# Kernel optimization log

Hardware: AMD Instinct MI355X
Metric: run time of the kernel (lower is better)

## Reference

```python
import jax, jax.numpy as jnp
import numpy as np

EPS = 1e-5

def _bn(x, g, b):
    # training-mode BatchNorm1d over the batch axis (axis 0), biased variance
    m = jnp.mean(x, axis=0)
    v = jnp.var(x, axis=0)
    return g * (x - m) / jnp.sqrt(v + EPS) + b

def _mlp(x, w1, b1, g1, be1, w2, b2, g2, be2, w3, b3):
    # Linear -> BN -> ReLU -> Linear -> BN -> ReLU -> Linear
    x = jax.nn.relu(_bn(x @ w1.T + b1, g1, be1))
    x = jax.nn.relu(_bn(x @ w2.T + b2, g2, be2))
    return x @ w3.T + b3

def setup_inputs() -> dict:
    key = jax.random.key(0)
    ks = jax.random.split(key, 10)
    B, S, D = 256, 512, 128
    w = lambda k: jax.random.normal(k, (D, D), jnp.float32) * 0.05
    return {
        "s": jax.random.normal(ks[0], (B, S, D), jnp.float32),
        "c": jax.random.normal(ks[1], (B, D), jnp.float32),
        "s_w1": w(ks[2]), "s_b1": jnp.zeros((D,), jnp.float32),
        "s_g1": jnp.ones((D,), jnp.float32), "s_be1": jnp.zeros((D,), jnp.float32),
        "s_w2": w(ks[3]), "s_b2": jnp.zeros((D,), jnp.float32),
        "s_g2": jnp.ones((D,), jnp.float32), "s_be2": jnp.zeros((D,), jnp.float32),
        "s_w3": w(ks[4]), "s_b3": jnp.zeros((D,), jnp.float32),
        "c_w1": w(ks[5]), "c_b1": jnp.zeros((D,), jnp.float32),
        "c_g1": jnp.ones((D,), jnp.float32), "c_be1": jnp.zeros((D,), jnp.float32),
        "c_w2": w(ks[6]), "c_b2": jnp.zeros((D,), jnp.float32),
        "c_g2": jnp.ones((D,), jnp.float32), "c_be2": jnp.zeros((D,), jnp.float32),
        "c_w3": w(ks[7]), "c_b3": jnp.zeros((D,), jnp.float32),
    }

def reference(s, c,
              s_w1, s_b1, s_g1, s_be1, s_w2, s_b2, s_g2, s_be2, s_w3, s_b3,
              c_w1, c_b1, c_g1, c_be1, c_w2, c_b2, c_g2, c_be2, c_w3, c_b3):
    # c_mlp: [B, D] -> [B, D] (BN over batch)
    c_out = _mlp(c, c_w1, c_b1, c_g1, c_be1, c_w2, c_b2, c_g2, c_be2, c_w3, c_b3)
    # s_mlp applied per sequence slice; BN stats over batch axis 0 only
    # (matches the torch loop where each s[:, i, :] gets its own BN stats).
    # s: [B, S, D]; _bn with axis=0 gives per-(slice, feature) stats.
    s_h = _mlp(s, s_w1, s_b1, s_g1, s_be1, s_w2, s_b2, s_g2, s_be2, s_w3, s_b3)
    s_out = s_h * c_out[:, None, :]          # context gate, [B, S, D]
    aggregated_c = jnp.max(s_out, axis=1)    # pooling == 'max', [B, D]
    return (s_out, aggregated_c)
```

## Files before the change

### kernel.cpp

```cpp
#include <hip/hip_runtime.h>
#include <hip/hip_bf16.h>
#include <math.h>

#define BATCH 256
#define SEQ   512
#define DIM   128
#define LDSK  136
#define LDSF  132

typedef __attribute__((ext_vector_type(8))) __bf16  bf16x8;
typedef __attribute__((ext_vector_type(4))) __bf16  bf16x4;
typedef __attribute__((ext_vector_type(4))) float   f32x4;

template<int RT>
__device__ __forceinline__ void matmul_layer(
    const __bf16* __restrict__ Xa, const __bf16* __restrict__ wg,
    const float* __restrict__ bias, f32x4 (&acc)[RT][8], int wave, int m, int q)
{
  const int rowbase = wave * RT * 16;
#pragma unroll
  for (int ct = 0; ct < 8; ++ct) {
    const float b = bias[ct * 16 + m];
    const f32x4 bv = {b, b, b, b};
#pragma unroll
    for (int rt = 0; rt < RT; ++rt) acc[rt][ct] = bv;
  }
#pragma unroll
  for (int ks = 0; ks < 4; ++ks) {
    const int k0 = ks * 32 + q * 8;
    bf16x8 a[RT];
#pragma unroll
    for (int rt = 0; rt < RT; ++rt)
      a[rt] = *(const bf16x8*)(Xa + (rowbase + rt * 16 + m) * LDSK + k0);
#pragma unroll
    for (int cg = 0; cg < 2; ++cg) {
      bf16x8 bw[4];
#pragma unroll
      for (int cj = 0; cj < 4; ++cj)
        bw[cj] = *(const bf16x8*)(wg + ((cg * 4 + cj) * 16 + m) * DIM + k0);
#pragma unroll
      for (int rt = 0; rt < RT; ++rt)
#pragma unroll
        for (int cj = 0; cj < 4; ++cj)
          acc[rt][cg * 4 + cj] =
              __builtin_amdgcn_mfma_f32_16x16x32_bf16(a[rt], bw[cj], acc[rt][cg * 4 + cj], 0, 0, 0);
    }
  }
}

template<int RT>
__device__ __forceinline__ void stats_accum(
    const f32x4 (&acc)[RT][8], float* sumL, float* sqL, int m, int q)
{
#pragma unroll
  for (int ct = 0; ct < 8; ++ct) {
    float s = 0.f, ss = 0.f;
#pragma unroll
    for (int rt = 0; rt < RT; ++rt)
#pragma unroll
      for (int r = 0; r < 4; ++r) { const float v = acc[rt][ct][r]; s += v; ss += v * v; }
    s  += __shfl_xor(s, 16, 64);  s  += __shfl_xor(s, 32, 64);
    ss += __shfl_xor(ss, 16, 64); ss += __shfl_xor(ss, 32, 64);
    if (q == 0) { atomicAdd(&sumL[ct * 16 + m], s); atomicAdd(&sqL[ct * 16 + m], ss); }
  }
}

template<int RT>
__device__ __forceinline__ void bn_relu_store(
    const f32x4 (&acc)[RT][8], __bf16* Xa, const float* sumL, const float* sqL,
    const float* __restrict__ g, const float* __restrict__ be,
    int wave, int m, int q)
{
  const int rowbase = wave * RT * 16;
#pragma unroll
  for (int ct = 0; ct < 8; ++ct) {
    const int n = ct * 16 + m;
    const float mean = sumL[n] * (1.0f / BATCH);
    const float var  = sqL[n]  * (1.0f / BATCH) - mean * mean;
    const float a = g[n] * rsqrtf(var + 1e-5f);
    const float c = be[n] - a * mean;
#pragma unroll
    for (int rt = 0; rt < RT; ++rt)
#pragma unroll
      for (int r = 0; r < 4; ++r) {
        const float y = fmaxf(0.f, a * acc[rt][ct][r] + c);
        const int row = rowbase + rt * 16 + q * 4 + r;
        Xa[row * LDSK + n] = (__bf16)y;
      }
  }
}

template<int NW, bool GATE>
__global__ __launch_bounds__(NW * 64, (NW == 8) ? 4 : 2)
void mlp_kernel(const float* __restrict__ xin, long xrow_stride,
                const __bf16* __restrict__ w1, const __bf16* __restrict__ w2,
                const __bf16* __restrict__ w3,
                const float* __restrict__ b1, const float* __restrict__ g1, const float* __restrict__ be1,
                const float* __restrict__ b2, const float* __restrict__ g2, const float* __restrict__ be2,
                const float* __restrict__ b3,
                const float* __restrict__ gate,
                float* __restrict__ out)
{
  const int tid  = threadIdx.x;
  constexpr int NT = NW * 64;
  constexpr int RT = 16 / NW;
  const int wave = tid >> 6, lane = tid & 63;
  const int m = lane & 15, q = lane >> 4;
  const int slice = GATE ? blockIdx.x : 0;
  const float* x0 = GATE ? (xin + (long)slice * DIM) : xin;

  __shared__ __align__(16) char XaRaw[BATCH * LDSK * 2];
  __bf16* Xa = (__bf16*)XaRaw;
  __shared__ float sum1[DIM], sq1[DIM], sum2[DIM], sq2[DIM];

  for (int t = tid; t < DIM; t += NT) { sum1[t] = 0.f; sq1[t] = 0.f; sum2[t] = 0.f; sq2[t] = 0.f; }

  {
    const int rpi = NT / 32;
    const int r0  = tid >> 5;
    const int c4  = (tid & 31) * 4;
#pragma unroll 4
    for (int it = 0; it < BATCH / rpi; ++it) {
      const int r = it * rpi + r0;
      const float4 v = *(const float4*)(x0 + (long)r * xrow_stride + c4);
      bf16x4 h = { (__bf16)v.x, (__bf16)v.y, (__bf16)v.z, (__bf16)v.w };
      *(bf16x4*)(Xa + r * LDSK + c4) = h;
    }
  }
  __syncthreads();

  f32x4 acc[RT][8];

  matmul_layer<RT>(Xa, w1, b1, acc, wave, m, q);
  stats_accum<RT>(acc, sum1, sq1, m, q);
  __syncthreads();
  bn_relu_store<RT>(acc, Xa, sum1, sq1, g1, be1, wave, m, q);

  matmul_layer<RT>(Xa, w2, b2, acc, wave, m, q);
  stats_accum<RT>(acc, sum2, sq2, m, q);
  __syncthreads();
  bn_relu_store<RT>(acc, Xa, sum2, sq2, g2, be2, wave, m, q);

  matmul_layer<RT>(Xa, w3, b3, acc, wave, m, q);

  if constexpr (GATE) {
    float* Xf = (float*)XaRaw;
    const int c4 = (tid & 31) * 4;
    const int r0 = tid >> 5;
    __syncthreads();
#pragma unroll
    for (int rt = 0; rt < RT; ++rt) {
#pragma unroll
      for (int ct = 0; ct < 8; ++ct)
#pragma unroll
        for (int r = 0; r < 4; ++r)
          Xf[(wave * 16 + q * 4 + r) * LDSF + ct * 16 + m] = acc[rt][ct][r];
      __syncthreads();
#pragma unroll 4
      for (int it = 0; it < 8; ++it) {
        const int crow = it * 16 + r0;
        const int grow = (crow >> 4) * 32 + rt * 16 + (crow & 15);
        float4 y = *(const float4*)(Xf + crow * LDSF + c4);
        const float4 gv = *(const float4*)(gate + grow * DIM + c4);
        y.x *= gv.x; y.y *= gv.y; y.z *= gv.z; y.w *= gv.w;
        *(float4*)(out + ((long)grow * SEQ + slice) * DIM + c4) = y;
      }
      if (rt + 1 < RT) __syncthreads();
    }
  } else {
    const int rowbase = wave * RT * 16;
#pragma unroll
    for (int ct = 0; ct < 8; ++ct) {
      const int col = ct * 16 + m;
#pragma unroll
      for (int rt = 0; rt < RT; ++rt) {
#pragma unroll
        for (int r = 0; r < 4; ++r) {
          const int row = rowbase + rt * 16 + q * 4 + r;
          out[row * DIM + col] = acc[rt][ct][r];
        }
      }
    }
  }
}

__global__ void prep_kernel(const float* __restrict__ w0, const float* __restrict__ w1,
                            const float* __restrict__ w2, const float* __restrict__ w3,
                            const float* __restrict__ w4, const float* __restrict__ w5,
                            __bf16* __restrict__ dst)
{
  const int idx = blockIdx.x * blockDim.x + threadIdx.x;
  const int mi  = idx >> 12;
  const int j   = (idx & 4095) * 4;
  const float* srcs[6] = {w0, w1, w2, w3, w4, w5};
  const float4 v = *(const float4*)(srcs[mi] + j);
  bf16x4 h = { (__bf16)v.x, (__bf16)v.y, (__bf16)v.z, (__bf16)v.w };
  *(bf16x4*)(dst + mi * 16384 + j) = h;
}

__global__ __launch_bounds__(1024) void maxpool_kernel(
    const float* __restrict__ sout, float* __restrict__ agg)
{
  __shared__ float4 red[1024];
  const int b = blockIdx.x;
  const int t = threadIdx.x;
  const int c4 = (t & 31) * 4, rg = t >> 5;
  const float* p = sout + (long)b * SEQ * DIM + c4;
  float4 mx = {-INFINITY, -INFINITY, -INFINITY, -INFINITY};
#pragma unroll 4
  for (int i = rg; i < SEQ; i += 32) {
    const float4 v = *(const float4*)(p + (long)i * DIM);
    mx.x = fmaxf(mx.x, v.x); mx.y = fmaxf(mx.y, v.y);
    mx.z = fmaxf(mx.z, v.z); mx.w = fmaxf(mx.w, v.w);
  }
  red[t] = mx;
  __syncthreads();
  if (t < 32) {
    float4 a = red[t];
#pragma unroll
    for (int k = 1; k < 32; ++k) {
      const float4 v = red[t + 32 * k];
      a.x = fmaxf(a.x, v.x); a.y = fmaxf(a.y, v.y);
      a.z = fmaxf(a.z, v.z); a.w = fmaxf(a.w, v.w);
    }
    *(float4*)(agg + b * DIM + c4) = a;
  }
}

extern "C" void kernel_launch(void* const* d_in, const int* in_sizes, int n_in,
                              void* d_out, int out_size, void* d_ws, size_t ws_size,
                              hipStream_t stream)
{
  const float* s     = (const float*)d_in[0];
  const float* c     = (const float*)d_in[1];
  const float* s_w1  = (const float*)d_in[2];
  const float* s_b1  = (const float*)d_in[3];
  const float* s_g1  = (const float*)d_in[4];
  const float* s_be1 = (const float*)d_in[5];
  const float* s_w2  = (const float*)d_in[6];
  const float* s_b2  = (const float*)d_in[7];
  const float* s_g2  = (const float*)d_in[8];
  const float* s_be2 = (const float*)d_in[9];
  const float* s_w3  = (const float*)d_in[10];
  const float* s_b3  = (const float*)d_in[11];
  const float* c_w1  = (const float*)d_in[12];
  const float* c_b1  = (const float*)d_in[13];
  const float* c_g1  = (const float*)d_in[14];
  const float* c_be1 = (const float*)d_in[15];
  const float* c_w2  = (const float*)d_in[16];
  const float* c_b2  = (const float*)d_in[17];
  const float* c_g2  = (const float*)d_in[18];
  const float* c_be2 = (const float*)d_in[19];
  const float* c_w3  = (const float*)d_in[20];
  const float* c_b3  = (const float*)d_in[21];

  float* out   = (float*)d_out;
  float* c_out = (float*)d_ws;
  __bf16* wbf  = (__bf16*)((char*)d_ws + (size_t)BATCH * DIM * sizeof(float));

  prep_kernel<<<96, 256, 0, stream>>>(s_w1, s_w2, s_w3, c_w1, c_w2, c_w3, wbf);

  mlp_kernel<16, false><<<1, 1024, 0, stream>>>(
      c, (long)DIM,
      wbf + 3 * 16384, wbf + 4 * 16384, wbf + 5 * 16384,
      c_b1, c_g1, c_be1, c_b2, c_g2, c_be2, c_b3,
      nullptr, c_out);

  mlp_kernel<8, true><<<SEQ, 512, 0, stream>>>(
      s, (long)SEQ * DIM,
      wbf, wbf + 16384, wbf + 2 * 16384,
      s_b1, s_g1, s_be1, s_b2, s_g2, s_be2, s_b3,
      c_out, out);

  maxpool_kernel<<<BATCH, 1024, 0, stream>>>(out, out + (long)BATCH * SEQ * DIM);
}
```

Baseline: 281.6 us.

## Use 4-wave blocks with more rows per wave, LDS params and double-buffered epilogue

Result: faster. 231.4 us (-17.8%).

```diff
diff --git a/kernel.cpp b/kernel.cpp
--- a/kernel.cpp
+++ b/kernel.cpp
@@ -15,7 +15,7 @@
 template<int RT>
 __device__ __forceinline__ void matmul_layer(
     const __bf16* __restrict__ Xa, const __bf16* __restrict__ wg,
-    const float* __restrict__ bias, f32x4 (&acc)[RT][8], int wave, int m, int q)
+    const float* bias, f32x4 (&acc)[RT][8], int wave, int m, int q)
 {
   const int rowbase = wave * RT * 16;
 #pragma unroll
@@ -28,23 +28,18 @@
 #pragma unroll
   for (int ks = 0; ks < 4; ++ks) {
     const int k0 = ks * 32 + q * 8;
-    bf16x8 a[RT];
+    bf16x8 a[RT], bw[8];
 #pragma unroll
     for (int rt = 0; rt < RT; ++rt)
       a[rt] = *(const bf16x8*)(Xa + (rowbase + rt * 16 + m) * LDSK + k0);
 #pragma unroll
-    for (int cg = 0; cg < 2; ++cg) {
-      bf16x8 bw[4];
-#pragma unroll
-      for (int cj = 0; cj < 4; ++cj)
-        bw[cj] = *(const bf16x8*)(wg + ((cg * 4 + cj) * 16 + m) * DIM + k0);
-#pragma unroll
-      for (int rt = 0; rt < RT; ++rt)
-#pragma unroll
-        for (int cj = 0; cj < 4; ++cj)
-          acc[rt][cg * 4 + cj] =
-              __builtin_amdgcn_mfma_f32_16x16x32_bf16(a[rt], bw[cj], acc[rt][cg * 4 + cj], 0, 0, 0);
-    }
+    for (int ct = 0; ct < 8; ++ct)
+      bw[ct] = *(const bf16x8*)(wg + (ct * 16 + m) * DIM + k0);
+#pragma unroll
+    for (int rt = 0; rt < RT; ++rt)
+#pragma unroll
+      for (int ct = 0; ct < 8; ++ct)
+        acc[rt][ct] = __builtin_amdgcn_mfma_f32_16x16x32_bf16(a[rt], bw[ct], acc[rt][ct], 0, 0, 0);
   }
 }
 
@@ -68,8 +63,7 @@
 template<int RT>
 __device__ __forceinline__ void bn_relu_store(
     const f32x4 (&acc)[RT][8], __bf16* Xa, const float* sumL, const float* sqL,
-    const float* __restrict__ g, const float* __restrict__ be,
-    int wave, int m, int q)
+    const float* g, const float* be, int wave, int m, int q)
 {
   const int rowbase = wave * RT * 16;
 #pragma unroll
@@ -91,7 +85,7 @@
 }
 
 template<int NW, bool GATE>
-__global__ __launch_bounds__(NW * 64, (NW == 8) ? 4 : 2)
+__global__ __launch_bounds__(NW * 64, 2)
 void mlp_kernel(const float* __restrict__ xin, long xrow_stride,
                 const __bf16* __restrict__ w1, const __bf16* __restrict__ w2,
                 const __bf16* __restrict__ w3,
@@ -112,14 +106,20 @@
   __shared__ __align__(16) char XaRaw[BATCH * LDSK * 2];
   __bf16* Xa = (__bf16*)XaRaw;
   __shared__ float sum1[DIM], sq1[DIM], sum2[DIM], sq2[DIM];
+  __shared__ float prm[7 * DIM];
 
   for (int t = tid; t < DIM; t += NT) { sum1[t] = 0.f; sq1[t] = 0.f; sum2[t] = 0.f; sq2[t] = 0.f; }
+  if (tid < DIM) {
+    prm[tid]           = b1[tid];  prm[DIM + tid]     = g1[tid];  prm[2 * DIM + tid] = be1[tid];
+    prm[3 * DIM + tid] = b2[tid];  prm[4 * DIM + tid] = g2[tid];  prm[5 * DIM + tid] = be2[tid];
+    prm[6 * DIM + tid] = b3[tid];
+  }
 
   {
     const int rpi = NT / 32;
     const int r0  = tid >> 5;
     const int c4  = (tid & 31) * 4;
-#pragma unroll 4
+#pragma unroll
     for (int it = 0; it < BATCH / rpi; ++it) {
       const int r = it * rpi + r0;
       const float4 v = *(const float4*)(x0 + (long)r * xrow_stride + c4);
@@ -131,41 +131,41 @@
 
   f32x4 acc[RT][8];
 
-  matmul_layer<RT>(Xa, w1, b1, acc, wave, m, q);
+  matmul_layer<RT>(Xa, w1, prm, acc, wave, m, q);
   stats_accum<RT>(acc, sum1, sq1, m, q);
   __syncthreads();
-  bn_relu_store<RT>(acc, Xa, sum1, sq1, g1, be1, wave, m, q);
-
-  matmul_layer<RT>(Xa, w2, b2, acc, wave, m, q);
+  bn_relu_store<RT>(acc, Xa, sum1, sq1, prm + DIM, prm + 2 * DIM, wave, m, q);
+
+  matmul_layer<RT>(Xa, w2, prm + 3 * DIM, acc, wave, m, q);
   stats_accum<RT>(acc, sum2, sq2, m, q);
   __syncthreads();
-  bn_relu_store<RT>(acc, Xa, sum2, sq2, g2, be2, wave, m, q);
-
-  matmul_layer<RT>(Xa, w3, b3, acc, wave, m, q);
+  bn_relu_store<RT>(acc, Xa, sum2, sq2, prm + 4 * DIM, prm + 5 * DIM, wave, m, q);
+
+  matmul_layer<RT>(Xa, w3, prm + 6 * DIM, acc, wave, m, q);
 
   if constexpr (GATE) {
     float* Xf = (float*)XaRaw;
-    const int c4 = (tid & 31) * 4;
-    const int r0 = tid >> 5;
+    const int c4l = (tid & 31) * 4;
+    const int r0  = tid >> 5;
     __syncthreads();
 #pragma unroll
     for (int rt = 0; rt < RT; ++rt) {
+      float* buf = Xf + (rt & 1) * 64 * LDSF;
 #pragma unroll
       for (int ct = 0; ct < 8; ++ct)
 #pragma unroll
         for (int r = 0; r < 4; ++r)
-          Xf[(wave * 16 + q * 4 + r) * LDSF + ct * 16 + m] = acc[rt][ct][r];
+          buf[(wave * 16 + q * 4 + r) * LDSF + ct * 16 + m] = acc[rt][ct][r];
       __syncthreads();
-#pragma unroll 4
+#pragma unroll
       for (int it = 0; it < 8; ++it) {
-        const int crow = it * 16 + r0;
-        const int grow = (crow >> 4) * 32 + rt * 16 + (crow & 15);
-        float4 y = *(const float4*)(Xf + crow * LDSF + c4);
-        const float4 gv = *(const float4*)(gate + grow * DIM + c4);
+        const int crow = it * 8 + r0;
+        const int grow = (crow >> 4) * 64 + rt * 16 + (crow & 15);
+        float4 y = *(const float4*)(buf + crow * LDSF + c4l);
+        const float4 gv = *(const float4*)(gate + grow * DIM + c4l);
         y.x *= gv.x; y.y *= gv.y; y.z *= gv.z; y.w *= gv.w;
-        *(float4*)(out + ((long)grow * SEQ + slice) * DIM + c4) = y;
+        *(float4*)(out + ((long)grow * SEQ + slice) * DIM + c4l) = y;
       }
-      if (rt + 1 < RT) __syncthreads();
     }
   } else {
     const int rowbase = wave * RT * 16;
@@ -260,13 +260,13 @@
 
   prep_kernel<<<96, 256, 0, stream>>>(s_w1, s_w2, s_w3, c_w1, c_w2, c_w3, wbf);
 
-  mlp_kernel<16, false><<<1, 1024, 0, stream>>>(
+  mlp_kernel<8, false><<<1, 512, 0, stream>>>(
       c, (long)DIM,
       wbf + 3 * 16384, wbf + 4 * 16384, wbf + 5 * 16384,
       c_b1, c_g1, c_be1, c_b2, c_g2, c_be2, c_b3,
       nullptr, c_out);
 
-  mlp_kernel<8, true><<<SEQ, 512, 0, stream>>>(
+  mlp_kernel<4, true><<<SEQ, 256, 0, stream>>>(
       s, (long)SEQ * DIM,
       wbf, wbf + 16384, wbf + 2 * 16384,
       s_b1, s_g1, s_be1, s_b2, s_g2, s_be2, s_b3,
```
